# Performance work log

Hardware: AMD Instinct MI355X
Metric: run time of the kernel (lower is better)

## Reference

```python
import jax, jax.numpy as jnp
import numpy as np

B, T, D, H = 4, 1024, 1024, 16
HD = D // H  # 64
EPS = 1e-5


def _layernorm(x, g, b):
    mu = jnp.mean(x, axis=-1, keepdims=True)
    var = jnp.mean(jnp.square(x - mu), axis=-1, keepdims=True)
    return (x - mu) * jax.lax.rsqrt(var + EPS) * g + b


def _apply_rope(x, cos, sin):
    # x: (B, H, T, HD); cos/sin: (T, HD//2)
    d = x.shape[-1] // 2
    x1, x2 = x[..., :d], x[..., d:]
    cos = cos[None, None]
    sin = sin[None, None]
    return jnp.concatenate([x1 * cos - x2 * sin, x1 * sin + x2 * cos], axis=-1)


def setup_inputs() -> dict:
    key = jax.random.key(0)
    ks = jax.random.split(key, 8)
    s = 0.02
    x = jax.random.normal(ks[0], (B, T, D), jnp.float32)
    # RoPE tables
    pos = jnp.arange(T, dtype=jnp.float32)
    inv_freq = 1.0 / (10000.0 ** (jnp.arange(HD // 2, dtype=jnp.float32) / (HD // 2)))
    ang = pos[:, None] * inv_freq[None, :]  # (T, HD//2)
    rope_cos, rope_sin = jnp.cos(ang), jnp.sin(ang)
    # causal mask: True = masked out (module does ~attn_mask before SDPA)
    attn_mask = jnp.triu(jnp.ones((T, T), dtype=bool), k=1)
    params = dict(
        ln1_g=jnp.ones((D,), jnp.float32), ln1_b=jnp.zeros((D,), jnp.float32),
        w_qkv=jax.random.normal(ks[1], (D, 3 * D), jnp.float32) * s,
        b_qkv=jnp.zeros((3 * D,), jnp.float32),
        w_out=jax.random.normal(ks[2], (D, D), jnp.float32) * s,
        b_out=jnp.zeros((D,), jnp.float32),
        ln2_g=jnp.ones((D,), jnp.float32), ln2_b=jnp.zeros((D,), jnp.float32),
        w1=jax.random.normal(ks[3], (D, 4 * D), jnp.float32) * s,
        b1=jnp.zeros((4 * D,), jnp.float32),
        w2=jax.random.normal(ks[4], (4 * D, D), jnp.float32) * s,
        b2=jnp.zeros((D,), jnp.float32),
    )
    return dict(x=x, attn_mask=attn_mask, rope_cos=rope_cos, rope_sin=rope_sin, **params)


def reference(x, attn_mask, rope_cos, rope_sin, ln1_g, ln1_b, w_qkv, b_qkv,
              w_out, b_out, ln2_g, ln2_b, w1, b1, w2, b2):
    b, t, d = x.shape
    h = _layernorm(x, ln1_g, ln1_b)
    qkv = (h @ w_qkv + b_qkv).reshape(b, t, 3, H, HD)
    q, k, v = jnp.transpose(qkv, (2, 0, 3, 1, 4))  # each (B, H, T, HD)
    q = _apply_rope(q, rope_cos, rope_sin)
    k = _apply_rope(k, rope_cos, rope_sin)
    scale = 1.0 / jnp.sqrt(jnp.asarray(HD, x.dtype))
    scores = jnp.einsum('bhqd,bhkd->bhqk', q, k) * scale
    allowed = ~attn_mask  # True = attend
    neg = jnp.finfo(scores.dtype).min
    scores = jnp.where(allowed[None, None], scores, neg)
    probs = jax.nn.softmax(scores, axis=-1)
    attn = jnp.einsum('bhqk,bhkd->bhqd', probs, v)
    attn = jnp.transpose(attn, (0, 2, 1, 3)).reshape(b, t, d)
    x = x + (attn @ w_out + b_out)
    h2 = _layernorm(x, ln2_g, ln2_b)
    mlp = jax.nn.gelu(h2 @ w1 + b1, approximate=False) @ w2 + b2
    return x + mlp
```

## Files before the change

### kernel.cpp

```cpp
#include <hip/hip_runtime.h>
#include <hip/hip_bf16.h>
#include <cstdint>


typedef __bf16 bf16x8_t __attribute__((ext_vector_type(8)));
typedef float  f32x4_t  __attribute__((ext_vector_type(4)));

#define MFMA16(a, b, c) __builtin_amdgcn_mfma_f32_16x16x32_bf16((a), (b), (c), 0, 0, 0)

static constexpr int Bb = 4, T = 1024, D = 1024, NH = 16, HD = 64;
static constexpr int ROWS = Bb * T;
static constexpr int QKVN = 3 * D;

__device__ __forceinline__ float bf2f(__hip_bfloat16 v) { return __bfloat162float(v); }
__device__ __forceinline__ ushort f2bfbits(float v) {
    __hip_bfloat16 h = __float2bfloat16(v);
    return *reinterpret_cast<ushort*>(&h);
}
__device__ __forceinline__ float loadf(const void* p, size_t i, int isb16) {
    return isb16 ? bf2f(((const __hip_bfloat16*)p)[i]) : ((const float*)p)[i];
}
__device__ __forceinline__ int dtype16(const void* gref) {
    return (((const unsigned*)gref)[0] & 0xFFFFu) != 0u;
}
__device__ __forceinline__ void gld_lds16(const __hip_bfloat16* g, __hip_bfloat16* l) {
    __builtin_amdgcn_global_load_lds(
        (const __attribute__((address_space(1))) void*)g,
        (__attribute__((address_space(3))) void*)l, 16, 0, 0);
}

__device__ __forceinline__ int xcd_swz(int id0, int nwg) {
    return (id0 & 7) * (nwg >> 3) + (id0 >> 3);
}

__device__ __forceinline__ void trans_tile_core(ushort* sc, const void* B,
                                                __hip_bfloat16* BT,
                                                int K, int N, int k0, int n0, int isb16) {
#pragma unroll
    for (int it = 0; it < 4; ++it) {
        int gi = threadIdx.x + it * 256;
        int r = gi >> 4, c4 = (gi & 15) * 4;
        if (isb16) {
            ushort4 v = *reinterpret_cast<const ushort4*>(
                (const __hip_bfloat16*)B + (size_t)(k0 + r) * N + n0 + c4);
            sc[(c4 + 0) * 68 + r] = v.x; sc[(c4 + 1) * 68 + r] = v.y;
            sc[(c4 + 2) * 68 + r] = v.z; sc[(c4 + 3) * 68 + r] = v.w;
        } else {
            float4 v = *reinterpret_cast<const float4*>(
                (const float*)B + (size_t)(k0 + r) * N + n0 + c4);
            sc[(c4 + 0) * 68 + r] = f2bfbits(v.x); sc[(c4 + 1) * 68 + r] = f2bfbits(v.y);
            sc[(c4 + 2) * 68 + r] = f2bfbits(v.z); sc[(c4 + 3) * 68 + r] = f2bfbits(v.w);
        }
    }
    __syncthreads();
#pragma unroll
    for (int it = 0; it < 4; ++it) {
        int gi = threadIdx.x + it * 256;
        int r = gi >> 4, c4 = (gi & 15) * 4;
        ushort4 v = *reinterpret_cast<const ushort4*>(&sc[r * 68 + c4]);
        *reinterpret_cast<ushort4*>(
            reinterpret_cast<ushort*>(BT) + (size_t)(n0 + r) * K + k0 + c4) = v;
    }
}

__device__ __forceinline__ void trans_tile(const void* B, __hip_bfloat16* BT,
                                           int K, int N, int k0, int n0, int isb16) {
    __shared__ ushort t[64 * 68];
    trans_tile_core(t, B, BT, K, N, k0, n0, isb16);
}

__device__ __forceinline__ void ln_row(const void* x, const void* g, const void* bt,
                                       __hip_bfloat16* out, int row, int isb16) {
    const int tid = threadIdx.x;
    const int lane = tid & 63, w = tid >> 6;

    float v[4];
    if (isb16) {
        ushort4 raw = reinterpret_cast<const ushort4*>((const __hip_bfloat16*)x + (size_t)row * D)[tid];
        v[0] = __uint_as_float(((unsigned)raw.x) << 16);
        v[1] = __uint_as_float(((unsigned)raw.y) << 16);
        v[2] = __uint_as_float(((unsigned)raw.z) << 16);
        v[3] = __uint_as_float(((unsigned)raw.w) << 16);
    } else {
        float4 f = reinterpret_cast<const float4*>((const float*)x + (size_t)row * D)[tid];
        v[0] = f.x; v[1] = f.y; v[2] = f.z; v[3] = f.w;
    }

    float s1 = v[0] + v[1] + v[2] + v[3];
    float s2 = v[0] * v[0] + v[1] * v[1] + v[2] * v[2] + v[3] * v[3];
#pragma unroll
    for (int off = 32; off >= 1; off >>= 1) {
        s1 += __shfl_xor(s1, off, 64);
        s2 += __shfl_xor(s2, off, 64);
    }
    __shared__ float r1[4], r2[4];
    if (lane == 0) { r1[w] = s1; r2[w] = s2; }
    __syncthreads();
    float t1 = r1[0] + r1[1] + r1[2] + r1[3];
    float t2 = r2[0] + r2[1] + r2[2] + r2[3];
    float mu  = t1 * (1.0f / D);
    float var = t2 * (1.0f / D) - mu * mu;
    float rstd = rsqrtf(var + 1e-5f);

    const int c = tid * 4;
    float gv[4], bv[4];
    if (isb16) {
        ushort4 gg = *reinterpret_cast<const ushort4*>((const __hip_bfloat16*)g + c);
        ushort4 bb = *reinterpret_cast<const ushort4*>((const __hip_bfloat16*)bt + c);
        gv[0] = __uint_as_float((unsigned)gg.x << 16); gv[1] = __uint_as_float((unsigned)gg.y << 16);
        gv[2] = __uint_as_float((unsigned)gg.z << 16); gv[3] = __uint_as_float((unsigned)gg.w << 16);
        bv[0] = __uint_as_float((unsigned)bb.x << 16); bv[1] = __uint_as_float((unsigned)bb.y << 16);
        bv[2] = __uint_as_float((unsigned)bb.z << 16); bv[3] = __uint_as_float((unsigned)bb.w << 16);
    } else {
        float4 gg = *reinterpret_cast<const float4*>((const float*)g + c);
        float4 bb = *reinterpret_cast<const float4*>((const float*)bt + c);
        gv[0] = gg.x; gv[1] = gg.y; gv[2] = gg.z; gv[3] = gg.w;
        bv[0] = bb.x; bv[1] = bb.y; bv[2] = bb.z; bv[3] = bb.w;
    }
    ushort4 o;
    o.x = f2bfbits((v[0] - mu) * rstd * gv[0] + bv[0]);
    o.y = f2bfbits((v[1] - mu) * rstd * gv[1] + bv[1]);
    o.z = f2bfbits((v[2] - mu) * rstd * gv[2] + bv[2]);
    o.w = f2bfbits((v[3] - mu) * rstd * gv[3] + bv[3]);
    *reinterpret_cast<ushort4*>(out + (size_t)row * D + c) = o;
}

__global__ __launch_bounds__(256) void transpose_k(const void* __restrict__ B,
                                                   __hip_bfloat16* __restrict__ BT,
                                                   const void* __restrict__ gref,
                                                   int K, int N) {
    trans_tile(B, BT, K, N, blockIdx.y * 64, blockIdx.x * 64, dtype16(gref));
}

__global__ __launch_bounds__(256) void fusedpre_k(const void* w_qkv,
                                                  __hip_bfloat16* wqkvT,
                                                  const void* __restrict__ x,
                                                  const void* __restrict__ ln_g,
                                                  const void* __restrict__ ln_b,
                                                  __hip_bfloat16* __restrict__ ln_out,
                                                  const void* __restrict__ gref) {
    const int isb16 = dtype16(gref);
    int bid = blockIdx.x;
    if (bid < 768) {
        const int nb = QKVN / 64;
        trans_tile(w_qkv, wqkvT, D, QKVN, (bid / nb) * 64, (bid % nb) * 64, isb16);
    } else {
        ln_row(x, ln_g, ln_b, ln_out, bid - 768, isb16);
    }
}

__global__ __launch_bounds__(256) void ln_k(const void* __restrict__ x,
                                            const void* __restrict__ g,
                                            const void* __restrict__ bt,
                                            __hip_bfloat16* __restrict__ out,
                                            const void* __restrict__ gref) {
    ln_row(x, g, bt, out, blockIdx.x, dtype16(gref));
}

template <int MODE, bool SPLIT>
__global__ __launch_bounds__(512, 2) void gemm256_k(const __hip_bfloat16* __restrict__ A,
                                                    const __hip_bfloat16* __restrict__ BT,
                                                    const void* __restrict__ bias,
                                                    void* __restrict__ C,
                                                    const void* __restrict__ gref,
                                                    int M, int N, int Kstride, int klen) {
    extern __shared__ __hip_bfloat16 LDSb[];

    const int tid  = threadIdx.x;
    const int lane = tid & 63, w = tid >> 6;
    const int quad = lane >> 4, l15 = lane & 15;

    const int gx = gridDim.x;
    const int sid = xcd_swz((int)blockIdx.y * gx + (int)blockIdx.x, gx * (int)gridDim.y);
    const int n0 = (sid % gx) * 256, m0 = (sid / gx) * 256;

    const int wmL = (w >> 2) * 128;
    const int wnL = (w & 3) * 64;
    const int kbase = SPLIT ? blockIdx.z * klen : 0;
    const int NT = klen >> 5;

    const int L0 = w * 1024 + lane * 16;
    const int L1 = L0 + 8192;
    const int r0 = L0 >> 6,  k0e = ((L0 & 63) ^ (((L0 >> 9) & 1) << 5)) >> 1;
    const int r1 = L1 >> 6,  k1e = ((L1 & 63) ^ (((L1 >> 9) & 1) << 5)) >> 1;
    const __hip_bfloat16* AgS0 = A  + (size_t)(m0 + r0) * Kstride + kbase + k0e;
    const __hip_bfloat16* AgS1 = A  + (size_t)(m0 + r1) * Kstride + kbase + k1e;
    const __hip_bfloat16* BgS0 = BT + (size_t)(n0 + r0) * Kstride + kbase + k0e;
    const __hip_bfloat16* BgS1 = BT + (size_t)(n0 + r1) * Kstride + kbase + k1e;
    const int ldst0 = w * 512, ldst1 = w * 512 + 4096;

    const int kofs = (quad * 8) ^ ((l15 & 8) << 1);

    f32x4_t acc[8][4] = {};

#pragma unroll
    for (int t = 0; t < 3; ++t) {
        __hip_bfloat16* sA = LDSb + t * 8192;
        __hip_bfloat16* sB = LDSb + 32768 + t * 8192;
        const int ko = t * 32;
        gld_lds16(AgS0 + ko, sA + ldst0);
        gld_lds16(AgS1 + ko, sA + ldst1);
        gld_lds16(BgS0 + ko, sB + ldst0);
        gld_lds16(BgS1 + ko, sB + ldst1);
    }
    asm volatile("s_waitcnt vmcnt(8)" ::: "memory");
    __builtin_amdgcn_s_barrier();
    __builtin_amdgcn_sched_barrier(0);

    for (int t = 0; t < NT; ++t) {
        if (t) {
            if (t + 2 < NT)      { asm volatile("s_waitcnt vmcnt(8)" ::: "memory"); }
            else if (t + 1 < NT) { asm volatile("s_waitcnt vmcnt(4)" ::: "memory"); }
            else                 { asm volatile("s_waitcnt vmcnt(0)" ::: "memory"); }
            __builtin_amdgcn_s_barrier();
            __builtin_amdgcn_sched_barrier(0);
        }
        if (t + 3 < NT) {
            const int sl = (t + 3) & 3;
            __hip_bfloat16* sA = LDSb + sl * 8192;
            __hip_bfloat16* sB = LDSb + 32768 + sl * 8192;
            const int ko = (t + 3) * 32;
            gld_lds16(AgS0 + ko, sA + ldst0);
            gld_lds16(AgS1 + ko, sA + ldst1);
            gld_lds16(BgS0 + ko, sB + ldst0);
            gld_lds16(BgS1 + ko, sB + ldst1);
        }

        const __hip_bfloat16* sA = LDSb + (t & 3) * 8192;
        const __hip_bfloat16* sB = LDSb + 32768 + (t & 3) * 8192;
        bf16x8_t a[8], b[4];
#pragma unroll
        for (int mf = 0; mf < 8; ++mf)
            a[mf] = *reinterpret_cast<const bf16x8_t*>(&sA[(wmL + mf * 16 + l15) * 32 + kofs]);
#pragma unroll
        for (int nf = 0; nf < 4; ++nf)
            b[nf] = *reinterpret_cast<const bf16x8_t*>(&sB[(wnL + nf * 16 + l15) * 32 + kofs]);
        __builtin_amdgcn_s_setprio(1);
#pragma unroll
        for (int mf = 0; mf < 8; ++mf)
#pragma unroll
            for (int nf = 0; nf < 4; ++nf)
                acc[mf][nf] = MFMA16(a[mf], b[nf], acc[mf][nf]);
        __builtin_amdgcn_s_setprio(0);
    }

    __syncthreads();

    __hip_bfloat16* Cb;
    if constexpr (SPLIT) {
        const int z = blockIdx.z;
        if (z == 0)      Cb = (__hip_bfloat16*)C;
        else if (z == 1) Cb = (__hip_bfloat16*)C + (size_t)M * N;
        else if (z == 2) Cb = (__hip_bfloat16*)const_cast<void*>(bias);
        else             Cb = (__hip_bfloat16*)const_cast<void*>(gref);
    } else {
        Cb = (__hip_bfloat16*)C;
    }
    const int isb16 = (MODE == 3) ? 0 : dtype16(gref);
    __hip_bfloat16* E = LDSb;
#pragma unroll
    for (int nf = 0; nf < 4; ++nf) {
        const int cc = wnL + nf * 16 + l15;
        const float bsv = (MODE == 3) ? 0.0f : loadf(bias, n0 + cc, isb16);
#pragma unroll
        for (int mf = 0; mf < 8; ++mf) {
            const int rbase = wmL + mf * 16 + quad * 4;
#pragma unroll
            for (int r = 0; r < 4; ++r) {
                const int rr = rbase + r;
                float v = acc[mf][nf][r] + bsv;
                if constexpr (MODE == 2)
                    v = 0.5f * v * (1.0f + erff(v * 0.70710678118654752f));
                E[rr * 256 + ((cc + (((rr >> 2) & 15) << 4)) & 255)] = __float2bfloat16(v);
            }
        }
    }
    __syncthreads();
#pragma unroll
    for (int it = 0; it < 16; ++it) {
        const int r = it * 16 + (tid >> 5), c = (tid & 31) * 8;
        const int cs = (c + (((r >> 2) & 15) << 4)) & 255;
        uint4 d = *reinterpret_cast<const uint4*>(&E[r * 256 + cs]);
        *reinterpret_cast<uint4*>(&Cb[(size_t)(m0 + r) * N + n0 + c]) = d;
    }
}

template <int MODE, bool SPLIT>
__global__ __launch_bounds__(256) void gemm_k(const __hip_bfloat16* __restrict__ A,
                                              const __hip_bfloat16* __restrict__ BT,
                                              const void* __restrict__ bias,
                                              void* __restrict__ C,
                                              const void* __restrict__ gref,
                                              int M, int N, int Kstride, int klen,
                                              const void* __restrict__ rc,
                                              const void* __restrict__ rs,
                                              __hip_bfloat16* __restrict__ vT) {
    __shared__ __hip_bfloat16 LB[16384];

    const int tid  = threadIdx.x;
    const int lane = tid & 63, w = tid >> 6;
    const int quad = lane >> 4, l15 = lane & 15;

    const int gx = gridDim.x;
    const int sid = xcd_swz((int)blockIdx.y * gx + (int)blockIdx.x, gx * (int)gridDim.y);
    const int n0 = (sid % gx) * 128, m0 = (sid / gx) * 128;

    const int wm = (w >> 1) * 64, wn = (w & 1) * 64;
    const int kbase = SPLIT ? blockIdx.z * klen : 0;

    const int srow = lane >> 2, skk = (lane & 3) * 8;
    const __hip_bfloat16* Ag = A  + (size_t)(m0 + w * 16 + srow) * Kstride + kbase + skk;
    const __hip_bfloat16* Bg = BT + (size_t)(n0 + w * 16 + srow) * Kstride + kbase + skk;
    const int lwb = (w * 16) * 32;

    f32x4_t acc[4][4] = {};

    gld_lds16(Ag,                LB + lwb);
    gld_lds16(Ag + 64 * Kstride, LB + lwb + 64 * 32);
    gld_lds16(Bg,                LB + 8192 + lwb);
    gld_lds16(Bg + 64 * Kstride, LB + 8192 + lwb + 64 * 32);
    __syncthreads();

    int p = 0;
    for (int k0 = 0; k0 < klen; k0 += 32) {
        if (k0 + 32 < klen) {
            __hip_bfloat16* An = LB + (p ^ 1) * 4096;
            __hip_bfloat16* Bn = LB + 8192 + (p ^ 1) * 4096;
            gld_lds16(Ag + k0 + 32,                An + lwb);
            gld_lds16(Ag + k0 + 32 + 64 * Kstride, An + lwb + 64 * 32);
            gld_lds16(Bg + k0 + 32,                Bn + lwb);
            gld_lds16(Bg + k0 + 32 + 64 * Kstride, Bn + lwb + 64 * 32);
        }

        const __hip_bfloat16* Ac = LB + p * 4096;
        const __hip_bfloat16* Bc = LB + 8192 + p * 4096;
        bf16x8_t af[4], bfr[4];
#pragma unroll
        for (int t = 0; t < 4; t++) {
            af[t]  = *reinterpret_cast<const bf16x8_t*>(&Ac[(wm + t * 16 + l15) * 32 + quad * 8]);
            bfr[t] = *reinterpret_cast<const bf16x8_t*>(&Bc[(wn + t * 16 + l15) * 32 + quad * 8]);
        }
#pragma unroll
        for (int i = 0; i < 4; i++)
#pragma unroll
            for (int j = 0; j < 4; j++)
                acc[i][j] = MFMA16(af[i], bfr[j], acc[i][j]);

        __syncthreads();
        p ^= 1;
    }

    __hip_bfloat16* Cb;
    if constexpr (SPLIT) {
        const int z = blockIdx.z;
        if (z == 0)      Cb = (__hip_bfloat16*)C;
        else if (z == 1) Cb = (__hip_bfloat16*)C + (size_t)M * N;
        else if (z == 2) Cb = (__hip_bfloat16*)const_cast<void*>(bias);
        else             Cb = (__hip_bfloat16*)const_cast<void*>(gref);
    } else {
        Cb = (__hip_bfloat16*)C;
    }
    const int isb16 = (MODE == 3) ? 0 : dtype16(gref);
    __hip_bfloat16* E = LB;

    if constexpr (MODE == 1) {
        const int sec = n0 >> 10;
#pragma unroll
        for (int j = 0; j < 2; j++) {
            const int cc0 = wn + j * 16 + l15;
            const int cc2 = cc0 + 32;
            const float bs0 = loadf(bias, n0 + cc0, isb16);
            const float bs2 = loadf(bias, n0 + cc2, isb16);
            const int d = j * 16 + l15;
#pragma unroll
            for (int i = 0; i < 4; i++) {
                const int rbase = wm + i * 16 + quad * 4;
#pragma unroll
                for (int r = 0; r < 4; r++) {
                    const int rr = rbase + r;
                    float v0 = acc[i][j][r] + bs0;
                    float v2 = acc[i][j + 2][r] + bs2;
                    if (sec < 2) {
                        const int t = (m0 + rr) & (T - 1);
                        const float cv = loadf(rc, (size_t)t * 32 + d, isb16);
                        const float sv = loadf(rs, (size_t)t * 32 + d, isb16);
                        float o0 = v0 * cv - v2 * sv;
                        float o2 = v0 * sv + v2 * cv;
                        if (sec == 0) { o0 *= 0.125f; o2 *= 0.125f; }
                        v0 = o0; v2 = o2;
                    }
                    E[rr * 128 + ((cc0 + (((rr >> 2) & 7) << 4)) & 127)] = __float2bfloat16(v0);
                    E[rr * 128 + ((cc2 + (((rr >> 2) & 7) << 4)) & 127)] = __float2bfloat16(v2);
                }
            }
        }
    } else {
#pragma unroll
        for (int j = 0; j < 4; j++) {
            const int cc = wn + j * 16 + l15;
            const float bsv = (MODE == 3) ? 0.0f : loadf(bias, n0 + cc, isb16);
#pragma unroll
            for (int i = 0; i < 4; i++) {
                const int rbase = wm + i * 16 + quad * 4;
#pragma unroll
                for (int r = 0; r < 4; r++) {
                    const int rr = rbase + r;
                    float v = acc[i][j][r] + bsv;
                    if constexpr (MODE == 2)
                        v = 0.5f * v * (1.0f + erff(v * 0.70710678118654752f));
                    E[rr * 128 + ((cc + (((rr >> 2) & 7) << 4)) & 127)] = __float2bfloat16(v);
                }
            }
        }
    }
    __syncthreads();
#pragma unroll
    for (int it = 0; it < 8; it++) {
        const int r = it * 16 + (tid >> 4), c = (tid & 15) * 8;
        const int cs = (c + (((r >> 2) & 7) << 4)) & 127;
        uint4 d = *reinterpret_cast<const uint4*>(&E[r * 128 + cs]);
        *reinterpret_cast<uint4*>(&Cb[(size_t)(m0 + r) * N + n0 + c]) = d;
    }

    if constexpr (MODE == 1) {
        if (n0 >= 2 * D) {
            const int bq  = m0 >> 10;
            const int t0  = m0 & (T - 1);
            const int n0v = n0 - 2 * D;
#pragma unroll
            for (int it = 0; it < 8; ++it) {
                const int idx = tid + it * 256;
                const int f   = idx >> 4;
                const int tg  = (idx & 15) * 8;
                alignas(16) ushort pk[8];
#pragma unroll
                for (int kk = 0; kk < 8; ++kk) {
                    const int tt = tg + kk;
                    pk[kk] = reinterpret_cast<const ushort*>(E)[
                        tt * 128 + ((f + (((tt >> 2) & 7) << 4)) & 127)];
                }
                *reinterpret_cast<uint4*>(
                    &vT[((size_t)(bq * 1024 + n0v + f)) * T + t0 + tg]) =
                    *reinterpret_cast<const uint4*>(pk);
            }
        }
    }
}

__global__ __launch_bounds__(256) void reduce4_k(const __hip_bfloat16* __restrict__ p0,
                                                 const __hip_bfloat16* __restrict__ p1,
                                                 const __hip_bfloat16* __restrict__ p2,
                                                 const __hip_bfloat16* __restrict__ p3,
                                                 const void* __restrict__ bias,
                                                 const void* __restrict__ res,
                                                 void* __restrict__ out,
                                                 const void* __restrict__ gref) {
    const int isb16 = dtype16(gref);
    const size_t i = ((size_t)blockIdx.x * 256 + threadIdx.x) * 4;
    ushort4 a = *reinterpret_cast<const ushort4*>(p0 + i);
    ushort4 b = *reinterpret_cast<const ushort4*>(p1 + i);
    ushort4 c = *reinterpret_cast<const ushort4*>(p2 + i);
    ushort4 d = *reinterpret_cast<const ushort4*>(p3 + i);
    const int col = (int)(i & (D - 1));
    float v[4];
    v[0] = __uint_as_float((unsigned)a.x << 16) + __uint_as_float((unsigned)b.x << 16)
         + __uint_as_float((unsigned)c.x << 16) + __uint_as_float((unsigned)d.x << 16);
    v[1] = __uint_as_float((unsigned)a.y << 16) + __uint_as_float((unsigned)b.y << 16)
         + __uint_as_float((unsigned)c.y << 16) + __uint_as_float((unsigned)d.y << 16);
    v[2] = __uint_as_float((unsigned)a.z << 16) + __uint_as_float((unsigned)b.z << 16)
         + __uint_as_float((unsigned)c.z << 16) + __uint_as_float((unsigned)d.z << 16);
    v[3] = __uint_as_float((unsigned)a.w << 16) + __uint_as_float((unsigned)b.w << 16)
         + __uint_as_float((unsigned)c.w << 16) + __uint_as_float((unsigned)d.w << 16);
    float bv[4], rv[4];
    if (isb16) {
        ushort4 bb = *reinterpret_cast<const ushort4*>((const __hip_bfloat16*)bias + col);
        ushort4 rr = *reinterpret_cast<const ushort4*>((const __hip_bfloat16*)res + i);
        bv[0] = __uint_as_float((unsigned)bb.x << 16); bv[1] = __uint_as_float((unsigned)bb.y << 16);
        bv[2] = __uint_as_float((unsigned)bb.z << 16); bv[3] = __uint_as_float((unsigned)bb.w << 16);
        rv[0] = __uint_as_float((unsigned)rr.x << 16); rv[1] = __uint_as_float((unsigned)rr.y << 16);
        rv[2] = __uint_as_float((unsigned)rr.z << 16); rv[3] = __uint_as_float((unsigned)rr.w << 16);
    } else {
        float4 bb = *reinterpret_cast<const float4*>((const float*)bias + col);
        float4 rr = *reinterpret_cast<const float4*>((const float*)res + i);
        bv[0] = bb.x; bv[1] = bb.y; bv[2] = bb.z; bv[3] = bb.w;
        rv[0] = rr.x; rv[1] = rr.y; rv[2] = rr.z; rv[3] = rr.w;
    }
#pragma unroll
    for (int j = 0; j < 4; j++) v[j] += bv[j] + rv[j];
    if (isb16) {
        ushort4 o;
        o.x = f2bfbits(v[0]); o.y = f2bfbits(v[1]); o.z = f2bfbits(v[2]); o.w = f2bfbits(v[3]);
        *reinterpret_cast<ushort4*>((__hip_bfloat16*)out + i) = o;
    } else {
        float4 o = {v[0], v[1], v[2], v[3]};
        *reinterpret_cast<float4*>((float*)out + i) = o;
    }
}

__global__ __launch_bounds__(256) void gemm64_k(const __hip_bfloat16* __restrict__ A,
                                                const __hip_bfloat16* __restrict__ BT,
                                                const void* __restrict__ bias,
                                                const void* __restrict__ res,
                                                void* __restrict__ C,
                                                const void* __restrict__ gref,
                                                int M, int N, int K, int crow0) {
    __shared__ __hip_bfloat16 LB64[12288];

    const int tid  = threadIdx.x;
    const int lane = tid & 63, w = tid >> 6;
    const int quad = lane >> 4, l15 = lane & 15;

    const int gx = gridDim.x;
    const int sid = xcd_swz((int)blockIdx.y * gx + (int)blockIdx.x, gx * (int)gridDim.y);
    const int n0 = (sid % gx) * 64, m0 = (sid / gx) * 128;

    const int wm = (w >> 1) * 64, wn = (w & 1) * 32;

    const int srow = lane >> 2, skk = (lane & 3) * 8;
    const __hip_bfloat16* Ag = A  + (size_t)(m0 + w * 16 + srow) * K + skk;
    const __hip_bfloat16* Bg = BT + (size_t)(n0 + w * 16 + srow) * K + skk;
    const int lwb = (w * 16) * 32;

    f32x4_t acc[4][2] = {};

    gld_lds16(Ag,          LB64 + lwb);
    gld_lds16(Ag + 64 * K, LB64 + lwb + 64 * 32);
    gld_lds16(Bg,          LB64 + 8192 + lwb);
    __syncthreads();

    int p = 0;
    for (int k0 = 0; k0 < K; k0 += 32) {
        if (k0 + 32 < K) {
            __hip_bfloat16* An = LB64 + (p ^ 1) * 4096;
            __hip_bfloat16* Bn = LB64 + 8192 + (p ^ 1) * 2048;
            gld_lds16(Ag + k0 + 32,          An + lwb);
            gld_lds16(Ag + k0 + 32 + 64 * K, An + lwb + 64 * 32);
            gld_lds16(Bg + k0 + 32,          Bn + lwb);
        }

        const __hip_bfloat16* Ac = LB64 + p * 4096;
        const __hip_bfloat16* Bc = LB64 + 8192 + p * 2048;
        bf16x8_t af[4], bfr[2];
#pragma unroll
        for (int t = 0; t < 4; t++)
            af[t]  = *reinterpret_cast<const bf16x8_t*>(&Ac[(wm + t * 16 + l15) * 32 + quad * 8]);
#pragma unroll
        for (int t = 0; t < 2; t++)
            bfr[t] = *reinterpret_cast<const bf16x8_t*>(&Bc[(wn + t * 16 + l15) * 32 + quad * 8]);
#pragma unroll
        for (int i = 0; i < 4; i++)
#pragma unroll
            for (int j = 0; j < 2; j++)
                acc[i][j] = MFMA16(af[i], bfr[j], acc[i][j]);

        __syncthreads();
        p ^= 1;
    }

    const int isb16 = dtype16(gref);
    __hip_bfloat16* E = LB64;
#pragma unroll
    for (int j = 0; j < 2; j++) {
        const int cc = wn + j * 16 + l15;
        const float bsv = loadf(bias, n0 + cc, isb16);
#pragma unroll
        for (int i = 0; i < 4; i++) {
            const int rbase = wm + i * 16 + quad * 4;
#pragma unroll
            for (int r = 0; r < 4; r++) {
                const int rr = rbase + r;
                E[rr * 64 + ((cc + (((rr >> 2) & 7) << 4)) & 63)] =
                    __float2bfloat16(acc[i][j][r] + bsv);
            }
        }
    }
    __syncthreads();
#pragma unroll
    for (int it = 0; it < 4; it++) {
        const int r = it * 32 + (tid >> 3), c = (tid & 7) * 8;
        const int cs = (c + (((r >> 2) & 7) << 4)) & 63;
        const size_t gr = (size_t)(crow0 + m0 + r);
        alignas(16) ushort pk[8];
        *reinterpret_cast<uint4*>(pk) = *reinterpret_cast<const uint4*>(&E[r * 64 + cs]);
        if (isb16) {
            const ushort4 rv0 = *reinterpret_cast<const ushort4*>(
                (const __hip_bfloat16*)res + gr * N + n0 + c);
            const ushort4 rv1 = *reinterpret_cast<const ushort4*>(
                (const __hip_bfloat16*)res + gr * N + n0 + c + 4);
            const ushort rvs[8] = {rv0.x, rv0.y, rv0.z, rv0.w, rv1.x, rv1.y, rv1.z, rv1.w};
            alignas(16) ushort o[8];
#pragma unroll
            for (int k = 0; k < 8; k++)
                o[k] = f2bfbits(__uint_as_float((unsigned)pk[k] << 16) +
                                __uint_as_float((unsigned)rvs[k] << 16));
            *reinterpret_cast<uint4*>((__hip_bfloat16*)C + gr * N + n0 + c) =
                *reinterpret_cast<const uint4*>(o);
        } else {
            const float4 r0 = *reinterpret_cast<const float4*>(
                (const float*)res + gr * N + n0 + c);
            const float4 r1 = *reinterpret_cast<const float4*>(
                (const float*)res + gr * N + n0 + c + 4);
            const float rf[8] = {r0.x, r0.y, r0.z, r0.w, r1.x, r1.y, r1.z, r1.w};
            float ov[8];
#pragma unroll
            for (int k = 0; k < 8; k++)
                ov[k] = __uint_as_float((unsigned)pk[k] << 16) + rf[k];
            float4 s0 = {ov[0], ov[1], ov[2], ov[3]};
            float4 s1 = {ov[4], ov[5], ov[6], ov[7]};
            *reinterpret_cast<float4*>((float*)C + gr * N + n0 + c)     = s0;
            *reinterpret_cast<float4*>((float*)C + gr * N + n0 + c + 4) = s1;
        }
    }
}

__global__ __launch_bounds__(256) void ropevt_k(__hip_bfloat16* __restrict__ qkv,
                                                const void* __restrict__ rc,
                                                const void* __restrict__ rs,
                                                __hip_bfloat16* __restrict__ vT,
                                                const void* __restrict__ gref) {
    const int bid = blockIdx.x;
    if (bid < 8192) {
        const int isb16 = dtype16(gref);
        const int id = bid * 256 + threadIdx.x;
        const int d  = id & 31;
        const int h  = (id >> 5) & 15;
        const int t  = (id >> 9) & 1023;
        const int b  = id >> 19;
        const float c = loadf(rc, t * 32 + d, isb16);
        const float s = loadf(rs, t * 32 + d, isb16);
        __hip_bfloat16* base = qkv + ((size_t)(b * T + t)) * QKVN + h * HD + d;
        float x1 = bf2f(base[0]), x2 = bf2f(base[32]);
        base[0]  = __float2bfloat16((x1 * c - x2 * s) * 0.125f);
        base[32] = __float2bfloat16((x1 * s + x2 * c) * 0.125f);
        float y1 = bf2f(base[D]), y2 = bf2f(base[D + 32]);
        base[D]      = __float2bfloat16(y1 * c - y2 * s);
        base[D + 32] = __float2bfloat16(y1 * s + y2 * c);
    } else {
        __shared__ ushort t[64][65];
        const int l = bid - 8192;
        const int t0 = (l & 15) * 64, bh = l >> 4;
        const int b = bh >> 4, h = bh & 15;
        const __hip_bfloat16* src = qkv + ((size_t)b * T) * QKVN + 2 * D + h * HD;
#pragma unroll
        for (int it = 0; it < 16; ++it) {
            int idx = threadIdx.x + it * 256;
            int r = idx >> 6, d = idx & 63;
            t[d][r] = *reinterpret_cast<const ushort*>(src + (size_t)(t0 + r) * QKVN + d);
        }
        __syncthreads();
#pragma unroll
        for (int it = 0; it < 16; ++it) {
            int idx = threadIdx.x + it * 256;
            int r = idx >> 6, c = idx & 63;
            reinterpret_cast<ushort*>(vT)[((size_t)bh * 64 + r) * T + t0 + c] = t[r][c];
        }
    }
}

__global__ __launch_bounds__(256) void flash_k(const __hip_bfloat16* __restrict__ qkv,
                                               const __hip_bfloat16* __restrict__ vT,
                                               __hip_bfloat16* __restrict__ out,
                                               const void* __restrict__ w_out,
                                               const void* __restrict__ w1,
                                               const void* __restrict__ w2,
                                               __hip_bfloat16* __restrict__ woutT,
                                               __hip_bfloat16* __restrict__ w1T,
                                               __hip_bfloat16* __restrict__ w2T,
                                               const void* __restrict__ gref) {
    __shared__ __hip_bfloat16 FL[24576];
    const int tid = threadIdx.x;
    const int bid = blockIdx.x;

    if (bid >= 1024) {
        const int l = bid - 1024;
        const void* src; __hip_bfloat16* dst; int K, N, ll;
        if (l < 256)       { src = w_out; dst = woutT; K = 1024; N = 1024; ll = l; }
        else if (l < 1280) { src = w1;    dst = w1T;   K = 1024; N = 4096; ll = l - 256; }
        else               { src = w2;    dst = w2T;   K = 4096; N = 1024; ll = l - 1280; }
        const int nb = N / 64;
        trans_tile_core(reinterpret_cast<ushort*>(FL), src, dst, K, N,
                        (ll / nb) * 64, (ll % nb) * 64, dtype16(gref));
        return;
    }

    __hip_bfloat16* Qsb = FL;
    __hip_bfloat16* Ksb = FL + 4096;
    __hip_bfloat16* Vsb = FL + 12288;
    __hip_bfloat16* Psb = FL + 20480;

    const int qt = 15 - (bid >> 6);
    const int bh = bid & 63;
    const int b = bh >> 4, h = bh & 15;
    const int q0 = qt * 64;
    const int lane = tid & 63, w = tid >> 6, quad = lane >> 4, l15 = lane & 15;
    const int srow = lane >> 2, skk = (lane & 3) * 8;

    const __hip_bfloat16* qg = qkv + ((size_t)(b * T) + q0 + w * 16 + srow) * QKVN + h * HD + skk;
    const __hip_bfloat16* kg = qkv + ((size_t)(b * T) + w * 16 + srow) * QKVN + D + h * HD + skk;
    const __hip_bfloat16* vg = vT + ((size_t)bh * 64 + w * 16 + srow) * T + skk;

    gld_lds16(qg,      Qsb + (w * 16) * 32);
    gld_lds16(qg + 32, Qsb + 2048 + (w * 16) * 32);
    gld_lds16(kg,      Ksb + (w * 16) * 32);
    gld_lds16(kg + 32, Ksb + 2048 + (w * 16) * 32);
    gld_lds16(vg,      Vsb + (w * 16) * 32);
    gld_lds16(vg + 32, Vsb + 2048 + (w * 16) * 32);
    __syncthreads();

    const bf16x8_t aq0 = *reinterpret_cast<const bf16x8_t*>(&Qsb[(w * 16 + l15) * 32 + quad * 8]);
    const bf16x8_t aq1 = *reinterpret_cast<const bf16x8_t*>(&Qsb[2048 + (w * 16 + l15) * 32 + quad * 8]);

    float m_run[4], l_run[4];
    f32x4_t o[4] = {};
#pragma unroll
    for (int i = 0; i < 4; i++) { m_run[i] = -1e30f; l_run[i] = 0.0f; }

    int p = 0;
    for (int kt = 0; kt <= qt; kt++) {
        if (kt < qt) {
            const size_t ko = (size_t)(kt + 1) * 64;
            __hip_bfloat16* Kn = Ksb + (p ^ 1) * 4096;
            __hip_bfloat16* Vn = Vsb + (p ^ 1) * 4096;
            gld_lds16(kg + ko * QKVN,      Kn + (w * 16) * 32);
            gld_lds16(kg + ko * QKVN + 32, Kn + 2048 + (w * 16) * 32);
            gld_lds16(vg + ko,             Vn + (w * 16) * 32);
            gld_lds16(vg + ko + 32,        Vn + 2048 + (w * 16) * 32);
        }

        const __hip_bfloat16* Kc = Ksb + p * 4096;
        const __hip_bfloat16* Vc = Vsb + p * 4096;

        f32x4_t s[4];
#pragma unroll
        for (int c = 0; c < 4; c++) {
            f32x4_t z = {};
            bf16x8_t k0f = *reinterpret_cast<const bf16x8_t*>(&Kc[(c * 16 + l15) * 32 + quad * 8]);
            bf16x8_t k1f = *reinterpret_cast<const bf16x8_t*>(&Kc[2048 + (c * 16 + l15) * 32 + quad * 8]);
            z = MFMA16(aq0, k0f, z);
            z = MFMA16(aq1, k1f, z);
            s[c] = z;
        }

        if (kt == qt) {
#pragma unroll
            for (int c = 0; c < 4; c++)
#pragma unroll
                for (int i = 0; i < 4; i++) {
                    int rr = w * 16 + quad * 4 + i;
                    int cc = c * 16 + l15;
                    if (cc > rr) s[c][i] = -1e30f;
                }
        }

        float mnew[4], alpha[4];
#pragma unroll
        for (int i = 0; i < 4; i++) {
            float mx = fmaxf(fmaxf(s[0][i], s[1][i]), fmaxf(s[2][i], s[3][i]));
#pragma unroll
            for (int off = 1; off < 16; off <<= 1) mx = fmaxf(mx, __shfl_xor(mx, off, 64));
            mnew[i] = fmaxf(m_run[i], mx);
            alpha[i] = __expf(m_run[i] - mnew[i]);
            m_run[i] = mnew[i];
        }
#pragma unroll
        for (int c = 0; c < 4; c++)
#pragma unroll
            for (int i = 0; i < 4; i++) s[c][i] = __expf(s[c][i] - mnew[i]);
#pragma unroll
        for (int i = 0; i < 4; i++) {
            float sm = s[0][i] + s[1][i] + s[2][i] + s[3][i];
#pragma unroll
            for (int off = 1; off < 16; off <<= 1) sm += __shfl_xor(sm, off, 64);
            l_run[i] = l_run[i] * alpha[i] + sm;
#pragma unroll
            for (int od = 0; od < 4; od++) o[od][i] *= alpha[i];
        }

        __hip_bfloat16* Pw = Psb + w * 1024;
#pragma unroll
        for (int c = 0; c < 4; c++)
#pragma unroll
            for (int i = 0; i < 4; i++)
                Pw[(c >> 1) * 512 + (quad * 4 + i) * 32 + (c & 1) * 16 + l15] =
                    __float2bfloat16(s[c][i]);

        bf16x8_t ap0 = *reinterpret_cast<const bf16x8_t*>(&Pw[l15 * 32 + quad * 8]);
        bf16x8_t ap1 = *reinterpret_cast<const bf16x8_t*>(&Pw[512 + l15 * 32 + quad * 8]);
#pragma unroll
        for (int od = 0; od < 4; od++) {
            bf16x8_t v0f = *reinterpret_cast<const bf16x8_t*>(&Vc[(od * 16 + l15) * 32 + quad * 8]);
            bf16x8_t v1f = *reinterpret_cast<const bf16x8_t*>(&Vc[2048 + (od * 16 + l15) * 32 + quad * 8]);
            o[od] = MFMA16(ap0, v0f, o[od]);
            o[od] = MFMA16(ap1, v1f, o[od]);
        }

        __syncthreads();
        p ^= 1;
    }

    __hip_bfloat16* Eo = Psb;
#pragma unroll
    for (int od = 0; od < 4; od++) {
        const int cc = od * 16 + l15;
#pragma unroll
        for (int i = 0; i < 4; i++) {
            const int rr = w * 16 + quad * 4 + i;
            Eo[rr * 64 + ((cc + (((rr >> 2) & 7) << 4)) & 63)] =
                __float2bfloat16(o[od][i] / l_run[i]);
        }
    }
    __syncthreads();
#pragma unroll
    for (int it = 0; it < 2; ++it) {
        const int r = it * 32 + (tid >> 3), c = (tid & 7) * 8;
        const int cs = (c + (((r >> 2) & 7) << 4)) & 63;
        uint4 d = *reinterpret_cast<const uint4*>(&Eo[r * 64 + cs]);
        *reinterpret_cast<uint4*>(
            &out[((size_t)b * T + q0 + r) * D + h * HD + c]) = d;
    }
}

extern "C" void kernel_launch(void* const* d_in, const int* in_sizes, int n_in,
                              void* d_out, int out_size, void* d_ws, size_t ws_size,
                              hipStream_t stream) {
    const int o = (in_sizes[1] == T * (HD / 2)) ? 1 : 2;
    const void* x     = d_in[0];
    const void* rc    = d_in[o + 0];
    const void* rs    = d_in[o + 1];
    const void* ln1g  = d_in[o + 2];
    const void* ln1b  = d_in[o + 3];
    const void* w_qkv = d_in[o + 4];
    const void* b_qkv = d_in[o + 5];
    const void* w_out = d_in[o + 6];
    const void* b_out = d_in[o + 7];
    const void* ln2g  = d_in[o + 8];
    const void* ln2b  = d_in[o + 9];
    const void* w1    = d_in[o + 10];
    const void* b1    = d_in[o + 11];
    const void* w2    = d_in[o + 12];
    const void* b2    = d_in[o + 13];

    char* ws = (char*)d_ws;
    const size_t MB = 1024 * 1024;

    static bool attr_done = false;
    if (!attr_done) {
        hipFuncSetAttribute(reinterpret_cast<const void*>(&gemm256_k<2, false>),
                            hipFuncAttributeMaxDynamicSharedMemorySize, 131072);
        hipFuncSetAttribute(reinterpret_cast<const void*>(&gemm256_k<3, true>),
                            hipFuncAttributeMaxDynamicSharedMemorySize, 131072);
        attr_done = true;
    }

    if (ws_size >= 72 * MB + 256) {
        __hip_bfloat16* bufA  = (__hip_bfloat16*)(ws + 256);
        __hip_bfloat16* qkvb  = (__hip_bfloat16*)(ws + 8 * MB + 256);
        __hip_bfloat16* vTb   = (__hip_bfloat16*)(ws + 32 * MB + 256);
        __hip_bfloat16* mid   = qkvb;
        __hip_bfloat16* wqkvT = (__hip_bfloat16*)(ws + 40 * MB + 256);
        __hip_bfloat16* woutT = (__hip_bfloat16*)(ws + 46 * MB + 256);
        __hip_bfloat16* w1T   = (__hip_bfloat16*)(ws + 48 * MB + 256);
        __hip_bfloat16* w2T   = (__hip_bfloat16*)(ws + 56 * MB + 256);
        __hip_bfloat16* part0 = (__hip_bfloat16*)(ws + 40 * MB + 256);
        __hip_bfloat16* part2 = (__hip_bfloat16*)(ws + 64 * MB + 256);
        __hip_bfloat16* part1 = (__hip_bfloat16*)(ws + 48 * MB + 256);
        __hip_bfloat16* part3 = bufA;

        fusedpre_k<<<768 + ROWS, 256, 0, stream>>>(w_qkv, wqkvT,
                                                   x, ln1g, ln1b, bufA, ln1g);
        gemm_k<1, false><<<dim3(QKVN / 128, ROWS / 128), 256, 0, stream>>>(
            bufA, wqkvT, b_qkv, qkvb, ln1g, ROWS, QKVN, D, D, rc, rs, vTb);
        flash_k<<<1024 + 2304, 256, 0, stream>>>(qkvb, vTb, bufA,
                                                 w_out, w1, w2, woutT, w1T, w2T, ln1g);
        gemm64_k<<<dim3(D / 64, ROWS / 128), 256, 0, stream>>>(bufA, woutT, b_out, x,
                                                               d_out, ln1g, ROWS, D, D, 0);
        ln_k<<<ROWS, 256, 0, stream>>>(d_out, ln2g, ln2b, bufA, ln1g);
        gemm256_k<2, false><<<dim3(4 * D / 256, ROWS / 256), 512, 131072, stream>>>(
            bufA, w1T, b1, mid, ln1g, ROWS, 4 * D, D, D);
        gemm256_k<3, true><<<dim3(D / 256, ROWS / 256, 4), 512, 131072, stream>>>(
            mid, w2T, part2, part0, part3, ROWS, D, 4 * D, D);
        reduce4_k<<<(ROWS * D) / (256 * 4), 256, 0, stream>>>(part0, part1, part2, part3,
                                                              b2, d_out, d_out, ln1g);
    } else {
        __hip_bfloat16* bufA  = (__hip_bfloat16*)(ws + 256);
        __hip_bfloat16* qkvb  = (__hip_bfloat16*)(ws + 8 * MB + 256);
        __hip_bfloat16* wqkvT = (__hip_bfloat16*)(ws + 32 * MB + 256);
        __hip_bfloat16* vTb   = (__hip_bfloat16*)(ws + 32 * MB + 256);
        __hip_bfloat16* woutT = (__hip_bfloat16*)(ws + 8 * MB + 256);
        __hip_bfloat16* w1T   = (__hip_bfloat16*)(ws + 8 * MB + 256);
        __hip_bfloat16* w2T   = (__hip_bfloat16*)(ws + 16 * MB + 256);
        __hip_bfloat16* mid   = (__hip_bfloat16*)(ws + 24 * MB + 256);

        transpose_k<<<dim3(QKVN / 64, D / 64), 256, 0, stream>>>(w_qkv, wqkvT, ln1g, D, QKVN);
        ln_k<<<ROWS, 256, 0, stream>>>(x, ln1g, ln1b, bufA, ln1g);
        gemm_k<0, false><<<dim3(QKVN / 128, ROWS / 128), 256, 0, stream>>>(
            bufA, wqkvT, b_qkv, qkvb, ln1g, ROWS, QKVN, D, D, nullptr, nullptr, nullptr);
        ropevt_k<<<8192 + 1024, 256, 0, stream>>>(qkvb, rc, rs, vTb, ln1g);
        flash_k<<<1024, 256, 0, stream>>>(qkvb, vTb, bufA,
                                          nullptr, nullptr, nullptr,
                                          nullptr, nullptr, nullptr, ln1g);
        transpose_k<<<dim3(D / 64, D / 64), 256, 0, stream>>>(w_out, woutT, ln1g, D, D);
        gemm64_k<<<dim3(D / 64, ROWS / 128), 256, 0, stream>>>(bufA, woutT, b_out, x,
                                                               d_out, ln1g, ROWS, D, D, 0);
        ln_k<<<ROWS, 256, 0, stream>>>(d_out, ln2g, ln2b, bufA, ln1g);
        transpose_k<<<dim3(4 * D / 64, D / 64), 256, 0, stream>>>(w1, w1T, ln1g, D, 4 * D);
        transpose_k<<<dim3(D / 64, 4 * D / 64), 256, 0, stream>>>(w2, w2T, ln1g, 4 * D, D);
        for (int c = 0; c < 2; c++) {
            const int ro = c * 2048;
            gemm_k<2, false><<<dim3(4 * D / 128, 2048 / 128), 256, 0, stream>>>(
                bufA + (size_t)ro * D, w1T, b1, mid, ln1g, 2048, 4 * D, D, D,
                nullptr, nullptr, nullptr);
            gemm64_k<<<dim3(D / 64, 2048 / 128), 256, 0, stream>>>(mid, w2T, b2, d_out,
                                                                   d_out, ln1g, 2048, D, 4 * D, ro);
        }
    }
}
```

Measured before the change: 343.1 us.

## Process two query tiles per flash-attention block to reuse K/V loads

After: 347.3 us. Within noise of the previous version (+1.2%).

```diff
diff --git a/kernel.cpp b/kernel.cpp
--- a/kernel.cpp
+++ b/kernel.cpp
@@ -671,8 +671,8 @@
     const int tid = threadIdx.x;
     const int bid = blockIdx.x;
 
-    if (bid >= 1024) {
-        const int l = bid - 1024;
+    if (bid >= 512) {
+        const int l = bid - 512;
         const void* src; __hip_bfloat16* dst; int K, N, ll;
         if (l < 256)       { src = w_out; dst = woutT; K = 1024; N = 1024; ll = l; }
         else if (l < 1280) { src = w1;    dst = w1T;   K = 1024; N = 4096; ll = l - 256; }
@@ -688,10 +688,11 @@
     __hip_bfloat16* Vsb = FL + 12288;
     __hip_bfloat16* Psb = FL + 20480;
 
-    const int qt = 15 - (bid >> 6);
+    const int qp = 7 - (bid >> 6);
     const int bh = bid & 63;
     const int b = bh >> 4, h = bh & 15;
-    const int q0 = qt * 64;
+    const int q0 = qp * 128;
+    const int qt0 = 2 * qp, qt1 = 2 * qp + 1;
     const int lane = tid & 63, w = tid >> 6, quad = lane >> 4, l15 = lane & 15;
     const int srow = lane >> 2, skk = (lane & 3) * 8;
 
@@ -707,17 +708,26 @@
     gld_lds16(vg + 32, Vsb + 2048 + (w * 16) * 32);
     __syncthreads();
 
-    const bf16x8_t aq0 = *reinterpret_cast<const bf16x8_t*>(&Qsb[(w * 16 + l15) * 32 + quad * 8]);
-    const bf16x8_t aq1 = *reinterpret_cast<const bf16x8_t*>(&Qsb[2048 + (w * 16 + l15) * 32 + quad * 8]);
-
-    float m_run[4], l_run[4];
-    f32x4_t o[4] = {};
-#pragma unroll
-    for (int i = 0; i < 4; i++) { m_run[i] = -1e30f; l_run[i] = 0.0f; }
+    bf16x8_t aq[2][2];
+    aq[0][0] = *reinterpret_cast<const bf16x8_t*>(&Qsb[(w * 16 + l15) * 32 + quad * 8]);
+    aq[0][1] = *reinterpret_cast<const bf16x8_t*>(&Qsb[2048 + (w * 16 + l15) * 32 + quad * 8]);
+    __syncthreads();
+    gld_lds16(qg + (size_t)64 * QKVN,      Qsb + (w * 16) * 32);
+    gld_lds16(qg + (size_t)64 * QKVN + 32, Qsb + 2048 + (w * 16) * 32);
+    __syncthreads();
+    aq[1][0] = *reinterpret_cast<const bf16x8_t*>(&Qsb[(w * 16 + l15) * 32 + quad * 8]);
+    aq[1][1] = *reinterpret_cast<const bf16x8_t*>(&Qsb[2048 + (w * 16 + l15) * 32 + quad * 8]);
+
+    float m_run[2][4], l_run[2][4];
+    f32x4_t o[2][4] = {};
+#pragma unroll
+    for (int s = 0; s < 2; ++s)
+#pragma unroll
+        for (int i = 0; i < 4; ++i) { m_run[s][i] = -1e30f; l_run[s][i] = 0.0f; }
 
     int p = 0;
-    for (int kt = 0; kt <= qt; kt++) {
-        if (kt < qt) {
+    for (int kt = 0; kt <= qt1; kt++) {
+        if (kt < qt1) {
             const size_t ko = (size_t)(kt + 1) * 64;
             __hip_bfloat16* Kn = Ksb + (p ^ 1) * 4096;
             __hip_bfloat16* Vn = Vsb + (p ^ 1) * 4096;
@@ -730,68 +740,80 @@
         const __hip_bfloat16* Kc = Ksb + p * 4096;
         const __hip_bfloat16* Vc = Vsb + p * 4096;
 
-        f32x4_t s[4];
+        bf16x8_t kf[4][2];
 #pragma unroll
         for (int c = 0; c < 4; c++) {
-            f32x4_t z = {};
-            bf16x8_t k0f = *reinterpret_cast<const bf16x8_t*>(&Kc[(c * 16 + l15) * 32 + quad * 8]);
-            bf16x8_t k1f = *reinterpret_cast<const bf16x8_t*>(&Kc[2048 + (c * 16 + l15) * 32 + quad * 8]);
-            z = MFMA16(aq0, k0f, z);
-            z = MFMA16(aq1, k1f, z);
-            s[c] = z;
-        }
-
-        if (kt == qt) {
+            kf[c][0] = *reinterpret_cast<const bf16x8_t*>(&Kc[(c * 16 + l15) * 32 + quad * 8]);
+            kf[c][1] = *reinterpret_cast<const bf16x8_t*>(&Kc[2048 + (c * 16 + l15) * 32 + quad * 8]);
+        }
+
+        __hip_bfloat16* Pw = Psb + w * 1024;
+
+#pragma unroll
+        for (int s = 0; s < 2; ++s) {
+            const int dqt = (s == 0) ? qt0 : qt1;
+            if (s == 0 && kt > qt0) continue;
+
+            f32x4_t sv[4];
+#pragma unroll
+            for (int c = 0; c < 4; c++) {
+                f32x4_t z = {};
+                z = MFMA16(aq[s][0], kf[c][0], z);
+                z = MFMA16(aq[s][1], kf[c][1], z);
+                sv[c] = z;
+            }
+
+            if (kt == dqt) {
+#pragma unroll
+                for (int c = 0; c < 4; c++)
+#pragma unroll
+                    for (int i = 0; i < 4; i++) {
+                        int rr = w * 16 + quad * 4 + i;
+                        int cc = c * 16 + l15;
+                        if (cc > rr) sv[c][i] = -1e30f;
+                    }
+            }
+
+            float mnew[4], alpha[4];
+#pragma unroll
+            for (int i = 0; i < 4; i++) {
+                float mx = fmaxf(fmaxf(sv[0][i], sv[1][i]), fmaxf(sv[2][i], sv[3][i]));
+#pragma unroll
+                for (int off = 1; off < 16; off <<= 1) mx = fmaxf(mx, __shfl_xor(mx, off, 64));
+                mnew[i] = fmaxf(m_run[s][i], mx);
+                alpha[i] = __expf(m_run[s][i] - mnew[i]);
+                m_run[s][i] = mnew[i];
+            }
 #pragma unroll
             for (int c = 0; c < 4; c++)
 #pragma unroll
-                for (int i = 0; i < 4; i++) {
-                    int rr = w * 16 + quad * 4 + i;
-                    int cc = c * 16 + l15;
-                    if (cc > rr) s[c][i] = -1e30f;
-                }
-        }
-
-        float mnew[4], alpha[4];
-#pragma unroll
-        for (int i = 0; i < 4; i++) {
-            float mx = fmaxf(fmaxf(s[0][i], s[1][i]), fmaxf(s[2][i], s[3][i]));
-#pragma unroll
-            for (int off = 1; off < 16; off <<= 1) mx = fmaxf(mx, __shfl_xor(mx, off, 64));
-            mnew[i] = fmaxf(m_run[i], mx);
-            alpha[i] = __expf(m_run[i] - mnew[i]);
-            m_run[i] = mnew[i];
-        }
-#pragma unroll
-        for (int c = 0; c < 4; c++)
-#pragma unroll
-            for (int i = 0; i < 4; i++) s[c][i] = __expf(s[c][i] - mnew[i]);
-#pragma unroll
-        for (int i = 0; i < 4; i++) {
-            float sm = s[0][i] + s[1][i] + s[2][i] + s[3][i];
-#pragma unroll
-            for (int off = 1; off < 16; off <<= 1) sm += __shfl_xor(sm, off, 64);
-            l_run[i] = l_run[i] * alpha[i] + sm;
-#pragma unroll
-            for (int od = 0; od < 4; od++) o[od][i] *= alpha[i];
-        }
-
-        __hip_bfloat16* Pw = Psb + w * 1024;
-#pragma unroll
-        for (int c = 0; c < 4; c++)
-#pragma unroll
-            for (int i = 0; i < 4; i++)
-                Pw[(c >> 1) * 512 + (quad * 4 + i) * 32 + (c & 1) * 16 + l15] =
-                    __float2bfloat16(s[c][i]);
-
-        bf16x8_t ap0 = *reinterpret_cast<const bf16x8_t*>(&Pw[l15 * 32 + quad * 8]);
-        bf16x8_t ap1 = *reinterpret_cast<const bf16x8_t*>(&Pw[512 + l15 * 32 + quad * 8]);
-#pragma unroll
-        for (int od = 0; od < 4; od++) {
-            bf16x8_t v0f = *reinterpret_cast<const bf16x8_t*>(&Vc[(od * 16 + l15) * 32 + quad * 8]);
-            bf16x8_t v1f = *reinterpret_cast<const bf16x8_t*>(&Vc[2048 + (od * 16 + l15) * 32 + quad * 8]);
-            o[od] = MFMA16(ap0, v0f, o[od]);
-            o[od] = MFMA16(ap1, v1f, o[od]);
+                for (int i = 0; i < 4; i++) sv[c][i] = __expf(sv[c][i] - mnew[i]);
+#pragma unroll
+            for (int i = 0; i < 4; i++) {
+                float sm = sv[0][i] + sv[1][i] + sv[2][i] + sv[3][i];
+#pragma unroll
+                for (int off = 1; off < 16; off <<= 1) sm += __shfl_xor(sm, off, 64);
+                l_run[s][i] = l_run[s][i] * alpha[i] + sm;
+#pragma unroll
+                for (int od = 0; od < 4; od++) o[s][od][i] *= alpha[i];
+            }
+
+#pragma unroll
+            for (int c = 0; c < 4; c++)
+#pragma unroll
+                for (int i = 0; i < 4; i++)
+                    Pw[(c >> 1) * 512 + (quad * 4 + i) * 32 + (c & 1) * 16 + l15] =
+                        __float2bfloat16(sv[c][i]);
+
+            bf16x8_t ap0 = *reinterpret_cast<const bf16x8_t*>(&Pw[l15 * 32 + quad * 8]);
+            bf16x8_t ap1 = *reinterpret_cast<const bf16x8_t*>(&Pw[512 + l15 * 32 + quad * 8]);
+#pragma unroll
+            for (int od = 0; od < 4; od++) {
+                bf16x8_t v0f = *reinterpret_cast<const bf16x8_t*>(&Vc[(od * 16 + l15) * 32 + quad * 8]);
+                bf16x8_t v1f = *reinterpret_cast<const bf16x8_t*>(&Vc[2048 + (od * 16 + l15) * 32 + quad * 8]);
+                o[s][od] = MFMA16(ap0, v0f, o[s][od]);
+                o[s][od] = MFMA16(ap1, v1f, o[s][od]);
+            }
         }
 
         __syncthreads();
@@ -800,23 +822,27 @@
 
     __hip_bfloat16* Eo = Psb;
 #pragma unroll
-    for (int od = 0; od < 4; od++) {
-        const int cc = od * 16 + l15;
-#pragma unroll
-        for (int i = 0; i < 4; i++) {
-            const int rr = w * 16 + quad * 4 + i;
-            Eo[rr * 64 + ((cc + (((rr >> 2) & 7) << 4)) & 63)] =
-                __float2bfloat16(o[od][i] / l_run[i]);
-        }
-    }
-    __syncthreads();
-#pragma unroll
-    for (int it = 0; it < 2; ++it) {
-        const int r = it * 32 + (tid >> 3), c = (tid & 7) * 8;
-        const int cs = (c + (((r >> 2) & 7) << 4)) & 63;
-        uint4 d = *reinterpret_cast<const uint4*>(&Eo[r * 64 + cs]);
-        *reinterpret_cast<uint4*>(
-            &out[((size_t)b * T + q0 + r) * D + h * HD + c]) = d;
+    for (int s = 0; s < 2; ++s) {
+#pragma unroll
+        for (int od = 0; od < 4; od++) {
+            const int cc = od * 16 + l15;
+#pragma unroll
+            for (int i = 0; i < 4; i++) {
+                const int rr = w * 16 + quad * 4 + i;
+                Eo[rr * 64 + ((cc + (((rr >> 2) & 7) << 4)) & 63)] =
+                    __float2bfloat16(o[s][od][i] / l_run[s][i]);
+            }
+        }
+        __syncthreads();
+#pragma unroll
+        for (int it = 0; it < 2; ++it) {
+            const int r = it * 32 + (tid >> 3), c = (tid & 7) * 8;
+            const int cs = (c + (((r >> 2) & 7) << 4)) & 63;
+            uint4 d = *reinterpret_cast<const uint4*>(&Eo[r * 64 + cs]);
+            *reinterpret_cast<uint4*>(
+                &out[((size_t)b * T + q0 + s * 64 + r) * D + h * HD + c]) = d;
+        }
+        __syncthreads();
     }
 }
 
@@ -870,8 +896,8 @@
                                                    x, ln1g, ln1b, bufA, ln1g);
         gemm_k<1, false><<<dim3(QKVN / 128, ROWS / 128), 256, 0, stream>>>(
             bufA, wqkvT, b_qkv, qkvb, ln1g, ROWS, QKVN, D, D, rc, rs, vTb);
-        flash_k<<<1024 + 2304, 256, 0, stream>>>(qkvb, vTb, bufA,
-                                                 w_out, w1, w2, woutT, w1T, w2T, ln1g);
+        flash_k<<<512 + 2304, 256, 0, stream>>>(qkvb, vTb, bufA,
+                                                w_out, w1, w2, woutT, w1T, w2T, ln1g);
         gemm64_k<<<dim3(D / 64, ROWS / 128), 256, 0, stream>>>(bufA, woutT, b_out, x,
                                                                d_out, ln1g, ROWS, D, D, 0);
         ln_k<<<ROWS, 256, 0, stream>>>(d_out, ln2g, ln2b, bufA, ln1g);
@@ -896,9 +922,9 @@
         gemm_k<0, false><<<dim3(QKVN / 128, ROWS / 128), 256, 0, stream>>>(
             bufA, wqkvT, b_qkv, qkvb, ln1g, ROWS, QKVN, D, D, nullptr, nullptr, nullptr);
         ropevt_k<<<8192 + 1024, 256, 0, stream>>>(qkvb, rc, rs, vTb, ln1g);
-        flash_k<<<1024, 256, 0, stream>>>(qkvb, vTb, bufA,
-                                          nullptr, nullptr, nullptr,
-                                          nullptr, nullptr, nullptr, ln1g);
+        flash_k<<<512, 256, 0, stream>>>(qkvb, vTb, bufA,
+                                         nullptr, nullptr, nullptr,
+                                         nullptr, nullptr, nullptr, ln1g);
         transpose_k<<<dim3(D / 64, D / 64), 256, 0, stream>>>(w_out, woutT, ln1g, D, D);
         gemm64_k<<<dim3(D / 64, ROWS / 128), 256, 0, stream>>>(bufA, woutT, b_out, x,
                                                                d_out, ln1g, ROWS, D, D, 0);
```
